# Performance work log

Measured on AMD Instinct MI355X. Metric: run time of the kernel, lower is better.

## Reference

```python
import jax, jax.numpy as jnp
import numpy as np

B, L, S, D, H, DH = 32, 96, 96, 512, 8, 64  # d_ff = S*S = 9216


def setup_inputs() -> dict:
    key = jax.random.key(0)
    ks = jax.random.split(key, 13)
    sc = 0.02
    inp = {
        "queries": jax.random.normal(ks[0], (B, L, D), jnp.float32),
        "keys": jax.random.normal(ks[1], (B, S, D), jnp.float32),
        "values": jax.random.normal(ks[2], (B, S, D), jnp.float32),
        "attn_mask": jnp.zeros((B, L, S), dtype=bool),
        # projections stored as (in, out); torch Linear is x @ W.T + b
        "Wq": jax.random.normal(ks[3], (D, H * DH), jnp.float32) * sc,
        "bq": jnp.zeros((H * DH,), jnp.float32),
        "Wk": jax.random.normal(ks[4], (D, H * DH), jnp.float32) * sc,
        "bk": jnp.zeros((H * DH,), jnp.float32),
        "Wv": jax.random.normal(ks[5], (D, H * DH), jnp.float32) * sc,
        "bv": jnp.zeros((H * DH,), jnp.float32),
        # core_value initialized as softmax over rank dim, as in the module
        "core": jax.nn.softmax(jax.random.normal(ks[6], (H, DH), jnp.float32), axis=-1),
        "Wo": jax.random.normal(ks[7], (S * S, D), jnp.float32) * sc,
        "bo": jnp.zeros((D,), jnp.float32),
    }
    return inp


def reference(queries, keys, values, attn_mask, Wq, bq, Wk, bk, Wv, bv, core, Wo, bo):
    b, l, _ = queries.shape
    s = keys.shape[1]
    h, d = core.shape
    # NOTE: the original uses .view(H, B, L, -1) on a (B, L, H*d) tensor —
    # a raw reshape, NOT a transpose. Replicate faithfully.
    q = (queries @ Wq + bq).reshape(h, b, l, d)
    k = (keys @ Wk + bk).reshape(h, b, s, d)
    v = (values @ Wv + bv).reshape(h, b, s, d)
    # per-head rank-d CP contraction, summed over heads, averaged by 1/H
    full = jnp.einsum("nh,nbih,nbjh,nbkh->bijk", core, q, k, v) / h  # [B,L,S,S]
    full = full.reshape(b, l, s * s)
    out = full @ Wo + bo  # [B, L, D]
    return out
```

## Files before the change

### kernel.cpp

```cpp
#include <hip/hip_runtime.h>
#include <hip/hip_bf16.h>
#include <stdint.h>

using bf16 = __hip_bfloat16;
typedef float v4f __attribute__((ext_vector_type(4)));
typedef short short8 __attribute__((ext_vector_type(8)));


__device__ __forceinline__ void async_cp16(void* l, const void* g) {
  __builtin_amdgcn_global_load_lds(
      (const __attribute__((address_space(1))) void*)(uintptr_t)g,
      (__attribute__((address_space(3))) void*)(uintptr_t)l, 16, 0, 0);
}

__global__ __launch_bounds__(256) void transpose_f32_bf16(
    const float* __restrict__ src, bf16* __restrict__ dst, int K, int N) {
  __shared__ bf16 T[32][33];
  const int k0 = blockIdx.x * 32, n0 = blockIdx.y * 32;
  const int t = threadIdx.x;
  const int r = t >> 3, c = (t & 7) * 4;
  float4 v = *reinterpret_cast<const float4*>(src + (size_t)(k0 + r) * N + n0 + c);
  T[c + 0][r] = __float2bfloat16(v.x);
  T[c + 1][r] = __float2bfloat16(v.y);
  T[c + 2][r] = __float2bfloat16(v.z);
  T[c + 3][r] = __float2bfloat16(v.w);
  __syncthreads();
  union { uint2 u; bf16 h[4]; } o;
  o.h[0] = T[r][c + 0]; o.h[1] = T[r][c + 1];
  o.h[2] = T[r][c + 2]; o.h[3] = T[r][c + 3];
  *reinterpret_cast<uint2*>(dst + (size_t)(n0 + r) * K + k0 + c) = o.u;
}

#define PJ_LD 72

__global__ __launch_bounds__(256) void proj_mfma(
    const float* __restrict__ X0, const float* __restrict__ X1,
    const float* __restrict__ X2,
    const bf16* __restrict__ WT0, const bf16* __restrict__ WT1,
    const bf16* __restrict__ WT2,
    const float* __restrict__ b0, const float* __restrict__ b1,
    const float* __restrict__ b2, const float* __restrict__ core,
    bf16* __restrict__ O0, bf16* __restrict__ O1, bf16* __restrict__ O2) {
  const int z = blockIdx.z;
  const float* X   = z == 0 ? X0  : (z == 1 ? X1  : X2);
  const bf16* WT   = z == 0 ? WT0 : (z == 1 ? WT1 : WT2);
  const float* bia = z == 0 ? b0  : (z == 1 ? b1  : b2);
  bf16* O          = z == 0 ? O0  : (z == 1 ? O1  : O2);

  __shared__ __align__(16) bf16 As[64 * PJ_LD];
  __shared__ __align__(16) bf16 Bs[64 * PJ_LD];
  const int t = threadIdx.x, w = t >> 6, lane = t & 63;
  const int wr = w >> 1, wc = w & 1, m16 = lane & 15, q = lane >> 4;
  const int bm = blockIdx.x * 64, bn = blockIdx.y * 64;

  v4f acc[2][2] = {};

  for (int k0 = 0; k0 < 512; k0 += 64) {
    __syncthreads();
    #pragma unroll
    for (int c = t; c < 1024; c += 256) {
      const int row = c >> 4, col = (c & 15) * 4;
      float4 v = *reinterpret_cast<const float4*>(
          X + (size_t)(bm + row) * 512 + k0 + col);
      union { uint2 u; bf16 h[4]; } o;
      o.h[0] = __float2bfloat16(v.x); o.h[1] = __float2bfloat16(v.y);
      o.h[2] = __float2bfloat16(v.z); o.h[3] = __float2bfloat16(v.w);
      *reinterpret_cast<uint2*>(&As[row * PJ_LD + col]) = o.u;
    }
    #pragma unroll
    for (int c = t; c < 512; c += 256) {
      const int row = c >> 3, col = (c & 7) * 8;
      *reinterpret_cast<uint4*>(&Bs[row * PJ_LD + col]) =
          *reinterpret_cast<const uint4*>(WT + (size_t)(bn + row) * 512 + k0 + col);
    }
    __syncthreads();

    #pragma unroll
    for (int s = 0; s < 2; s++) {
      const int koff = s * 32 + q * 8;
      short8 af[2], bfr[2];
      #pragma unroll
      for (int mt = 0; mt < 2; mt++)
        af[mt] = *reinterpret_cast<const short8*>(
            &As[(wr * 32 + mt * 16 + m16) * PJ_LD + koff]);
      #pragma unroll
      for (int nt = 0; nt < 2; nt++)
        bfr[nt] = *reinterpret_cast<const short8*>(
            &Bs[(wc * 32 + nt * 16 + m16) * PJ_LD + koff]);
      #pragma unroll
      for (int mt = 0; mt < 2; mt++)
        #pragma unroll
        for (int nt = 0; nt < 2; nt++)
          acc[mt][nt] = __builtin_amdgcn_mfma_f32_16x16x32_bf16(
              af[mt], bfr[nt], acc[mt][nt], 0, 0, 0);
    }
  }

  const bool isQ = (z == 0);
  const int nblk = bm / 384;
  #pragma unroll
  for (int mt = 0; mt < 2; mt++)
    #pragma unroll
    for (int nt = 0; nt < 2; nt++)
      #pragma unroll
      for (int r = 0; r < 4; r++) {
        const int row = bm + wr * 32 + mt * 16 + q * 4 + r;
        const int col = bn + wc * 32 + nt * 16 + m16;
        float v = acc[mt][nt][r] + bia[col];
        if (isQ) v *= core[nblk * 64 + (col & 63)] * 0.125f;
        O[(size_t)row * 512 + col] = __float2bfloat16(v);
      }
}

__global__ __launch_bounds__(256) void stage_b_mfma(
    const bf16* __restrict__ AQ, const bf16* __restrict__ KPb,
    const bf16* __restrict__ VPb, bf16* __restrict__ FULL) {
  const int b = blockIdx.y;
  const int i0 = blockIdx.x * 2;

  __shared__ __align__(16) bf16 smem[19456];
  bf16* Ks0 = smem;
  bf16* Ks1 = smem + 6144;
  bf16* Vs  = smem + 12288;
  bf16* aqs = smem + 18432;

  const int t = threadIdx.x;
  const int w = t >> 6, lane = t & 63;
  const int wr = w >> 1, wc = w & 1;
  const int m16 = lane & 15, q = lane >> 4;
  const int l8 = lane >> 3, l7 = lane & 7;

  if (t < 128) {
    const int isel = t & 1, n = t >> 4, seg = (t >> 1) & 7;
    *reinterpret_cast<uint4*>(&aqs[isel * 512 + n * 64 + seg * 8]) =
        *reinterpret_cast<const uint4*>(
            AQ + (size_t)n * 196608 + b * 6144 + (i0 + isel) * 64 + seg * 8);
  }

  union U8 { uint4 u; bf16 h[8]; };
  const int colq = (t & 7) * 8;
  const int rowk = t >> 3;
  const int krow7 = rowk & 7;

  U8 kk[3];
  {
    const bf16* Kp = KPb + b * 6144;
    #pragma unroll
    for (int c3 = 0; c3 < 3; c3++)
      kk[c3].u = *reinterpret_cast<const uint4*>(Kp + (t + c3 * 256) * 8);
  }

  v4f acc[2][3][3] = {};

  for (int n = 0; n < 8; n++) {
    __syncthreads();
    const bf16* Vp = VPb + (size_t)n * 196608 + b * 6144;
    #pragma unroll
    for (int c = 0; c < 3; c++) {
      const int r0 = (w * 3 + c) * 8;
      async_cp16(&Vs[(w * 3 + c) * 512],
                 Vp + (r0 + l8) * 64 + (l7 ^ l8) * 8);
    }
    float a0f[8], a1f[8];
    {
      U8 a0, a1;
      a0.u = *reinterpret_cast<const uint4*>(&aqs[n * 64 + colq]);
      a1.u = *reinterpret_cast<const uint4*>(&aqs[512 + n * 64 + colq]);
      #pragma unroll
      for (int e = 0; e < 8; e++) {
        a0f[e] = __bfloat162float(a0.h[e]);
        a1f[e] = __bfloat162float(a1.h[e]);
      }
    }
    #pragma unroll
    for (int c3 = 0; c3 < 3; c3++) {
      U8 s0, s1;
      #pragma unroll
      for (int e = 0; e < 8; e++) {
        const float kv = __bfloat162float(kk[c3].h[e]);
        s0.h[e] = __float2bfloat16(kv * a0f[e]);
        s1.h[e] = __float2bfloat16(kv * a1f[e]);
      }
      const int phys = (rowk + 32 * c3) * 64 + (l7 ^ krow7) * 8;
      *reinterpret_cast<uint4*>(&Ks0[phys]) = s0.u;
      *reinterpret_cast<uint4*>(&Ks1[phys]) = s1.u;
    }
    __syncthreads();
    if (n < 7) {
      const bf16* Kp1 = KPb + (size_t)(n + 1) * 196608 + b * 6144;
      #pragma unroll
      for (int c3 = 0; c3 < 3; c3++)
        kk[c3].u = *reinterpret_cast<const uint4*>(Kp1 + (t + c3 * 256) * 8);
    }

    #pragma unroll
    for (int s = 0; s < 2; s++) {
      const int pc = ((s * 4 + q) ^ (m16 & 7)) * 8;
      short8 bfr[3], af0[3], af1[3];
      #pragma unroll
      for (int cc = 0; cc < 3; cc++)
        bfr[cc] = *reinterpret_cast<const short8*>(
            &Vs[(wc * 48 + cc * 16 + m16) * 64 + pc]);
      #pragma unroll
      for (int a = 0; a < 3; a++) {
        af0[a] = *reinterpret_cast<const short8*>(
            &Ks0[(wr * 48 + a * 16 + m16) * 64 + pc]);
        af1[a] = *reinterpret_cast<const short8*>(
            &Ks1[(wr * 48 + a * 16 + m16) * 64 + pc]);
      }
      #pragma unroll
      for (int a = 0; a < 3; a++)
        #pragma unroll
        for (int cc = 0; cc < 3; cc++) {
          acc[0][a][cc] = __builtin_amdgcn_mfma_f32_16x16x32_bf16(
              af0[a], bfr[cc], acc[0][a][cc], 0, 0, 0);
          acc[1][a][cc] = __builtin_amdgcn_mfma_f32_16x16x32_bf16(
              af1[a], bfr[cc], acc[1][a][cc], 0, 0, 0);
        }
    }
  }

  __syncthreads();
  #pragma unroll
  for (int isel = 0; isel < 2; isel++)
    #pragma unroll
    for (int a = 0; a < 3; a++)
      #pragma unroll
      for (int cc = 0; cc < 3; cc++) {
        const int j0 = wr * 48 + a * 16, k0c = wc * 48 + cc * 16;
        #pragma unroll
        for (int r = 0; r < 4; r++)
          smem[isel * 9216 + (j0 + q * 4 + r) * 96 + k0c + m16] =
              __float2bfloat16(acc[isel][a][cc][r]);
      }
  __syncthreads();
  const size_t obase = (size_t)(b * 96 + i0) * 9216;
  #pragma unroll
  for (int c = t; c < 2304; c += 256)
    *reinterpret_cast<uint4*>(FULL + obase + c * 8) =
        *reinterpret_cast<const uint4*>(&smem[c * 8]);
}

__global__ __launch_bounds__(256) void init_out(
    const float* __restrict__ bo, float* __restrict__ out) {
  const int idx = (blockIdx.x * 256 + threadIdx.x) * 4;
  *reinterpret_cast<float4*>(out + idx) =
      *reinterpret_cast<const float4*>(bo + (idx & 511));
}

__global__ __launch_bounds__(256) void stage_c_mfma(
    const bf16* __restrict__ FULL, const bf16* __restrict__ WoT,
    float* __restrict__ out) {
  const int bm = blockIdx.x * 128, bn = blockIdx.y * 64;
  const int kbase = blockIdx.z * 2304;
  __shared__ __align__(16) bf16 As[128 * 128];
  __shared__ __align__(16) bf16 Bs[64 * 128];
  const int t = threadIdx.x;
  const int w = t >> 6, lane = t & 63;
  const int m16 = lane & 15, q = lane >> 4;
  const int l16 = lane >> 4, l15 = lane & 15;

  v4f acc[2][4] = {};

  for (int k0 = kbase; k0 < kbase + 2304; k0 += 128) {
    __syncthreads();
    #pragma unroll
    for (int c = 0; c < 8; c++) {
      const int row = (w * 8 + c) * 4 + l16;
      const int lch = l15 ^ (row & 7);
      async_cp16(&As[(w * 8 + c) * 512],
                 FULL + (size_t)(bm + row) * 9216 + k0 + lch * 8);
    }
    #pragma unroll
    for (int c = 0; c < 4; c++) {
      const int row = (w * 4 + c) * 4 + l16;
      const int lch = l15 ^ (row & 7);
      async_cp16(&Bs[(w * 4 + c) * 512],
                 WoT + (size_t)(bn + row) * 9216 + k0 + lch * 8);
    }
    __syncthreads();

    #pragma unroll
    for (int s = 0; s < 4; s++) {
      const int pc = ((s * 4 + q) ^ (m16 & 7)) * 8;
      short8 af[2], bfr[4];
      #pragma unroll
      for (int mt = 0; mt < 2; mt++)
        af[mt] = *reinterpret_cast<const short8*>(
            &As[(w * 32 + mt * 16 + m16) * 128 + pc]);
      #pragma unroll
      for (int nt = 0; nt < 4; nt++)
        bfr[nt] = *reinterpret_cast<const short8*>(
            &Bs[(nt * 16 + m16) * 128 + pc]);
      #pragma unroll
      for (int mt = 0; mt < 2; mt++)
        #pragma unroll
        for (int nt = 0; nt < 4; nt++)
          acc[mt][nt] = __builtin_amdgcn_mfma_f32_16x16x32_bf16(
              af[mt], bfr[nt], acc[mt][nt], 0, 0, 0);
    }
  }

  #pragma unroll
  for (int mt = 0; mt < 2; mt++)
    #pragma unroll
    for (int nt = 0; nt < 4; nt++)
      #pragma unroll
      for (int r = 0; r < 4; r++) {
        const int row = bm + w * 32 + mt * 16 + q * 4 + r;
        const int col = bn + nt * 16 + m16;
        atomicAdd(&out[(size_t)row * 512 + col], acc[mt][nt][r]);
      }
}

extern "C" void kernel_launch(void* const* d_in, const int* in_sizes, int n_in,
                              void* d_out, int out_size, void* d_ws, size_t ws_size,
                              hipStream_t stream) {
  const float* queries = (const float*)d_in[0];
  const float* keys    = (const float*)d_in[1];
  const float* values  = (const float*)d_in[2];
  const float* Wq   = (const float*)d_in[4];
  const float* bq   = (const float*)d_in[5];
  const float* Wk   = (const float*)d_in[6];
  const float* bk   = (const float*)d_in[7];
  const float* Wv   = (const float*)d_in[8];
  const float* bv   = (const float*)d_in[9];
  const float* core = (const float*)d_in[10];
  const float* Wo   = (const float*)d_in[11];
  const float* bo   = (const float*)d_in[12];
  float* out = (float*)d_out;

  char* ws = (char*)d_ws;
  bf16* AQb = (bf16*)(ws);
  bf16* KPb = (bf16*)(ws + 3145728);
  bf16* VPb = (bf16*)(ws + 6291456);
  bf16* WTq = (bf16*)(ws + 9437184);
  bf16* WTk = (bf16*)(ws + 9961472);
  bf16* WTv = (bf16*)(ws + 10485760);
  bf16* WoT = (bf16*)(ws + 11010048);
  bf16* FULL = (bf16*)(ws + 20447232);

  const dim3 blk(256);

  transpose_f32_bf16<<<dim3(16, 16),  blk, 0, stream>>>(Wq, WTq, 512, 512);
  transpose_f32_bf16<<<dim3(16, 16),  blk, 0, stream>>>(Wk, WTk, 512, 512);
  transpose_f32_bf16<<<dim3(16, 16),  blk, 0, stream>>>(Wv, WTv, 512, 512);
  transpose_f32_bf16<<<dim3(288, 16), blk, 0, stream>>>(Wo, WoT, 9216, 512);

  proj_mfma<<<dim3(48, 8, 3), blk, 0, stream>>>(
      queries, keys, values, WTq, WTk, WTv, bq, bk, bv, core, AQb, KPb, VPb);

  stage_b_mfma<<<dim3(48, 32), blk, 0, stream>>>(AQb, KPb, VPb, FULL);

  init_out<<<dim3(1536), blk, 0, stream>>>(bo, out);
  stage_c_mfma<<<dim3(24, 8, 4), blk, 0, stream>>>(FULL, WoT, out);
}
```

Before: 224.0 us.

## Fuse QKV weight transposes into projection, restructure stage B and stage C tiling

Three separate weight-transpose launches are removed: the projection kernel now reads fp32 W directly and transposes into shared memory while converting to bf16. Stage B now builds the scaled-K tiles for two heads per barrier pair, reads V fragments straight from global memory into registers instead of through LDS, and sets an occupancy hint of 3 blocks. Stage C moves to 128x128 output tiles with a 64-wide K step and an 8-way K split. This trades fewer launches and barriers for more register pressure, uncoalesced scalar LDS stores in the projection, and more atomics in stage C.

```diff
diff --git a/kernel.cpp b/kernel.cpp
--- a/kernel.cpp
+++ b/kernel.cpp
@@ -36,16 +36,16 @@
 __global__ __launch_bounds__(256) void proj_mfma(
     const float* __restrict__ X0, const float* __restrict__ X1,
     const float* __restrict__ X2,
-    const bf16* __restrict__ WT0, const bf16* __restrict__ WT1,
-    const bf16* __restrict__ WT2,
+    const float* __restrict__ W0, const float* __restrict__ W1,
+    const float* __restrict__ W2,
     const float* __restrict__ b0, const float* __restrict__ b1,
     const float* __restrict__ b2, const float* __restrict__ core,
     bf16* __restrict__ O0, bf16* __restrict__ O1, bf16* __restrict__ O2) {
   const int z = blockIdx.z;
-  const float* X   = z == 0 ? X0  : (z == 1 ? X1  : X2);
-  const bf16* WT   = z == 0 ? WT0 : (z == 1 ? WT1 : WT2);
-  const float* bia = z == 0 ? b0  : (z == 1 ? b1  : b2);
-  bf16* O          = z == 0 ? O0  : (z == 1 ? O1  : O2);
+  const float* X   = z == 0 ? X0 : (z == 1 ? X1 : X2);
+  const float* W   = z == 0 ? W0 : (z == 1 ? W1 : W2);
+  const float* bia = z == 0 ? b0 : (z == 1 ? b1 : b2);
+  bf16* O          = z == 0 ? O0 : (z == 1 ? O1 : O2);
 
   __shared__ __align__(16) bf16 As[64 * PJ_LD];
   __shared__ __align__(16) bf16 Bs[64 * PJ_LD];
@@ -68,10 +68,14 @@
       *reinterpret_cast<uint2*>(&As[row * PJ_LD + col]) = o.u;
     }
     #pragma unroll
-    for (int c = t; c < 512; c += 256) {
-      const int row = c >> 3, col = (c & 7) * 8;
-      *reinterpret_cast<uint4*>(&Bs[row * PJ_LD + col]) =
-          *reinterpret_cast<const uint4*>(WT + (size_t)(bn + row) * 512 + k0 + col);
+    for (int c = t; c < 1024; c += 256) {
+      const int kr = c >> 4, nc = (c & 15) * 4;
+      float4 v = *reinterpret_cast<const float4*>(
+          W + (size_t)(k0 + kr) * 512 + bn + nc);
+      Bs[(nc + 0) * PJ_LD + kr] = __float2bfloat16(v.x);
+      Bs[(nc + 1) * PJ_LD + kr] = __float2bfloat16(v.y);
+      Bs[(nc + 2) * PJ_LD + kr] = __float2bfloat16(v.z);
+      Bs[(nc + 3) * PJ_LD + kr] = __float2bfloat16(v.w);
     }
     __syncthreads();
 
@@ -112,188 +116,189 @@
       }
 }
 
-__global__ __launch_bounds__(256) void stage_b_mfma(
+__global__ __launch_bounds__(256, 3) void stage_b_mfma(
     const bf16* __restrict__ AQ, const bf16* __restrict__ KPb,
     const bf16* __restrict__ VPb, bf16* __restrict__ FULL) {
   const int b = blockIdx.y;
   const int i0 = blockIdx.x * 2;
 
-  __shared__ __align__(16) bf16 smem[19456];
-  bf16* Ks0 = smem;
-  bf16* Ks1 = smem + 6144;
-  bf16* Vs  = smem + 12288;
-  bf16* aqs = smem + 18432;
-
+  __shared__ __align__(16) bf16 smem[25600];
+  bf16* aqs = smem + 24576;
+
+  const int t = threadIdx.x;
+  const int w = t >> 6, lane = t & 63;
+  const int wr = w >> 1, wc = w & 1;
+  const int m16 = lane & 15, q = lane >> 4;
+
+  if (t < 128) {
+    const int isel = t & 1, n = t >> 4, seg = (t >> 1) & 7;
+    *reinterpret_cast<uint4*>(&aqs[isel * 512 + n * 64 + seg * 8]) =
+        *reinterpret_cast<const uint4*>(
+            AQ + (size_t)n * 196608 + b * 6144 + (i0 + isel) * 64 + seg * 8);
+  }
+
+  union U8 { uint4 u; bf16 h[8]; };
+  const int colq = (t & 7) * 8;
+  const int rowk = t >> 3;
+  const int krow7 = rowk & 7;
+
+  U8 kk[2][3];
+  #pragma unroll
+  for (int nn = 0; nn < 2; nn++) {
+    const bf16* Kp = KPb + (size_t)nn * 196608 + b * 6144;
+    #pragma unroll
+    for (int c3 = 0; c3 < 3; c3++)
+      kk[nn][c3].u = *reinterpret_cast<const uint4*>(Kp + (t + c3 * 256) * 8);
+  }
+
+  v4f acc[2][3][3] = {};
+
+  for (int np = 0; np < 4; np++) {
+    __syncthreads();
+    #pragma unroll
+    for (int nn = 0; nn < 2; nn++) {
+      const int n = np * 2 + nn;
+      U8 a0, a1;
+      a0.u = *reinterpret_cast<const uint4*>(&aqs[n * 64 + colq]);
+      a1.u = *reinterpret_cast<const uint4*>(&aqs[512 + n * 64 + colq]);
+      bf16* Ks0 = smem + (0 * 2 + nn) * 6144;
+      bf16* Ks1 = smem + (1 * 2 + nn) * 6144;
+      #pragma unroll
+      for (int c3 = 0; c3 < 3; c3++) {
+        U8 s0, s1;
+        #pragma unroll
+        for (int e = 0; e < 8; e++) {
+          const float kv = __bfloat162float(kk[nn][c3].h[e]);
+          s0.h[e] = __float2bfloat16(kv * __bfloat162float(a0.h[e]));
+          s1.h[e] = __float2bfloat16(kv * __bfloat162float(a1.h[e]));
+        }
+        const int phys = (rowk + 32 * c3) * 64 + (colq / 8 ^ krow7) * 8;
+        *reinterpret_cast<uint4*>(&Ks0[phys]) = s0.u;
+        *reinterpret_cast<uint4*>(&Ks1[phys]) = s1.u;
+      }
+    }
+    __syncthreads();
+    if (np < 3) {
+      #pragma unroll
+      for (int nn = 0; nn < 2; nn++) {
+        const bf16* Kp = KPb + (size_t)(np * 2 + 2 + nn) * 196608 + b * 6144;
+        #pragma unroll
+        for (int c3 = 0; c3 < 3; c3++)
+          kk[nn][c3].u =
+              *reinterpret_cast<const uint4*>(Kp + (t + c3 * 256) * 8);
+      }
+    }
+
+    #pragma unroll
+    for (int nn = 0; nn < 2; nn++) {
+      const bf16* Vp = VPb + (size_t)(np * 2 + nn) * 196608 + b * 6144;
+      const bf16* Ks0 = smem + nn * 6144;
+      const bf16* Ks1 = smem + (2 + nn) * 6144;
+      uint4 vf[2][3];
+      #pragma unroll
+      for (int s = 0; s < 2; s++)
+        #pragma unroll
+        for (int cc = 0; cc < 3; cc++)
+          vf[s][cc] = *reinterpret_cast<const uint4*>(
+              Vp + (wc * 48 + cc * 16 + m16) * 64 + s * 32 + q * 8);
+      #pragma unroll
+      for (int s = 0; s < 2; s++) {
+        const int pc = ((s * 4 + q) ^ (m16 & 7)) * 8;
+        short8 af0[3], af1[3];
+        #pragma unroll
+        for (int a = 0; a < 3; a++) {
+          af0[a] = *reinterpret_cast<const short8*>(
+              &Ks0[(wr * 48 + a * 16 + m16) * 64 + pc]);
+          af1[a] = *reinterpret_cast<const short8*>(
+              &Ks1[(wr * 48 + a * 16 + m16) * 64 + pc]);
+        }
+        #pragma unroll
+        for (int a = 0; a < 3; a++)
+          #pragma unroll
+          for (int cc = 0; cc < 3; cc++) {
+            const short8 bv = *reinterpret_cast<const short8*>(&vf[s][cc]);
+            acc[0][a][cc] = __builtin_amdgcn_mfma_f32_16x16x32_bf16(
+                af0[a], bv, acc[0][a][cc], 0, 0, 0);
+            acc[1][a][cc] = __builtin_amdgcn_mfma_f32_16x16x32_bf16(
+                af1[a], bv, acc[1][a][cc], 0, 0, 0);
+          }
+      }
+    }
+  }
+
+  __syncthreads();
+  #pragma unroll
+  for (int isel = 0; isel < 2; isel++)
+    #pragma unroll
+    for (int a = 0; a < 3; a++)
+      #pragma unroll
+      for (int cc = 0; cc < 3; cc++) {
+        const int j0 = wr * 48 + a * 16, k0c = wc * 48 + cc * 16;
+        #pragma unroll
+        for (int r = 0; r < 4; r++)
+          smem[isel * 9216 + (j0 + q * 4 + r) * 96 + k0c + m16] =
+              __float2bfloat16(acc[isel][a][cc][r]);
+      }
+  __syncthreads();
+  const size_t obase = (size_t)(b * 96 + i0) * 9216;
+  #pragma unroll
+  for (int c = t; c < 2304; c += 256)
+    *reinterpret_cast<uint4*>(FULL + obase + c * 8) =
+        *reinterpret_cast<const uint4*>(&smem[c * 8]);
+}
+
+__global__ __launch_bounds__(256) void init_out(
+    const float* __restrict__ bo, float* __restrict__ out) {
+  const int idx = (blockIdx.x * 256 + threadIdx.x) * 4;
+  *reinterpret_cast<float4*>(out + idx) =
+      *reinterpret_cast<const float4*>(bo + (idx & 511));
+}
+
+__global__ __launch_bounds__(256) void stage_c_mfma(
+    const bf16* __restrict__ FULL, const bf16* __restrict__ WoT,
+    float* __restrict__ out) {
+  const int bm = blockIdx.x * 128, bn = blockIdx.y * 128;
+  const int kbase = blockIdx.z * 1152;
+  __shared__ __align__(16) bf16 As[128 * 64];
+  __shared__ __align__(16) bf16 Bs[128 * 64];
   const int t = threadIdx.x;
   const int w = t >> 6, lane = t & 63;
   const int wr = w >> 1, wc = w & 1;
   const int m16 = lane & 15, q = lane >> 4;
   const int l8 = lane >> 3, l7 = lane & 7;
 
-  if (t < 128) {
-    const int isel = t & 1, n = t >> 4, seg = (t >> 1) & 7;
-    *reinterpret_cast<uint4*>(&aqs[isel * 512 + n * 64 + seg * 8]) =
-        *reinterpret_cast<const uint4*>(
-            AQ + (size_t)n * 196608 + b * 6144 + (i0 + isel) * 64 + seg * 8);
-  }
-
-  union U8 { uint4 u; bf16 h[8]; };
-  const int colq = (t & 7) * 8;
-  const int rowk = t >> 3;
-  const int krow7 = rowk & 7;
-
-  U8 kk[3];
-  {
-    const bf16* Kp = KPb + b * 6144;
-    #pragma unroll
-    for (int c3 = 0; c3 < 3; c3++)
-      kk[c3].u = *reinterpret_cast<const uint4*>(Kp + (t + c3 * 256) * 8);
-  }
-
-  v4f acc[2][3][3] = {};
-
-  for (int n = 0; n < 8; n++) {
-    __syncthreads();
-    const bf16* Vp = VPb + (size_t)n * 196608 + b * 6144;
-    #pragma unroll
-    for (int c = 0; c < 3; c++) {
-      const int r0 = (w * 3 + c) * 8;
-      async_cp16(&Vs[(w * 3 + c) * 512],
-                 Vp + (r0 + l8) * 64 + (l7 ^ l8) * 8);
-    }
-    float a0f[8], a1f[8];
-    {
-      U8 a0, a1;
-      a0.u = *reinterpret_cast<const uint4*>(&aqs[n * 64 + colq]);
-      a1.u = *reinterpret_cast<const uint4*>(&aqs[512 + n * 64 + colq]);
-      #pragma unroll
-      for (int e = 0; e < 8; e++) {
-        a0f[e] = __bfloat162float(a0.h[e]);
-        a1f[e] = __bfloat162float(a1.h[e]);
-      }
-    }
-    #pragma unroll
-    for (int c3 = 0; c3 < 3; c3++) {
-      U8 s0, s1;
-      #pragma unroll
-      for (int e = 0; e < 8; e++) {
-        const float kv = __bfloat162float(kk[c3].h[e]);
-        s0.h[e] = __float2bfloat16(kv * a0f[e]);
-        s1.h[e] = __float2bfloat16(kv * a1f[e]);
-      }
-      const int phys = (rowk + 32 * c3) * 64 + (l7 ^ krow7) * 8;
-      *reinterpret_cast<uint4*>(&Ks0[phys]) = s0.u;
-      *reinterpret_cast<uint4*>(&Ks1[phys]) = s1.u;
-    }
-    __syncthreads();
-    if (n < 7) {
-      const bf16* Kp1 = KPb + (size_t)(n + 1) * 196608 + b * 6144;
-      #pragma unroll
-      for (int c3 = 0; c3 < 3; c3++)
-        kk[c3].u = *reinterpret_cast<const uint4*>(Kp1 + (t + c3 * 256) * 8);
-    }
+  v4f acc[4][4] = {};
+
+  for (int k0 = kbase; k0 < kbase + 1152; k0 += 64) {
+    __syncthreads();
+    #pragma unroll
+    for (int c = 0; c < 4; c++) {
+      const int row = w * 32 + c * 8 + l8;
+      async_cp16(&As[(w * 4 + c) * 512],
+                 FULL + (size_t)(bm + row) * 9216 + k0 + (l7 ^ l8) * 8);
+    }
+    #pragma unroll
+    for (int c = 0; c < 4; c++) {
+      const int row = w * 32 + c * 8 + l8;
+      async_cp16(&Bs[(w * 4 + c) * 512],
+                 WoT + (size_t)(bn + row) * 9216 + k0 + (l7 ^ l8) * 8);
+    }
+    __syncthreads();
 
     #pragma unroll
     for (int s = 0; s < 2; s++) {
       const int pc = ((s * 4 + q) ^ (m16 & 7)) * 8;
-      short8 bfr[3], af0[3], af1[3];
-      #pragma unroll
-      for (int cc = 0; cc < 3; cc++)
-        bfr[cc] = *reinterpret_cast<const short8*>(
-            &Vs[(wc * 48 + cc * 16 + m16) * 64 + pc]);
-      #pragma unroll
-      for (int a = 0; a < 3; a++) {
-        af0[a] = *reinterpret_cast<const short8*>(
-            &Ks0[(wr * 48 + a * 16 + m16) * 64 + pc]);
-        af1[a] = *reinterpret_cast<const short8*>(
-            &Ks1[(wr * 48 + a * 16 + m16) * 64 + pc]);
-      }
-      #pragma unroll
-      for (int a = 0; a < 3; a++)
-        #pragma unroll
-        for (int cc = 0; cc < 3; cc++) {
-          acc[0][a][cc] = __builtin_amdgcn_mfma_f32_16x16x32_bf16(
-              af0[a], bfr[cc], acc[0][a][cc], 0, 0, 0);
-          acc[1][a][cc] = __builtin_amdgcn_mfma_f32_16x16x32_bf16(
-              af1[a], bfr[cc], acc[1][a][cc], 0, 0, 0);
-        }
-    }
-  }
-
-  __syncthreads();
-  #pragma unroll
-  for (int isel = 0; isel < 2; isel++)
-    #pragma unroll
-    for (int a = 0; a < 3; a++)
-      #pragma unroll
-      for (int cc = 0; cc < 3; cc++) {
-        const int j0 = wr * 48 + a * 16, k0c = wc * 48 + cc * 16;
-        #pragma unroll
-        for (int r = 0; r < 4; r++)
-          smem[isel * 9216 + (j0 + q * 4 + r) * 96 + k0c + m16] =
-              __float2bfloat16(acc[isel][a][cc][r]);
-      }
-  __syncthreads();
-  const size_t obase = (size_t)(b * 96 + i0) * 9216;
-  #pragma unroll
-  for (int c = t; c < 2304; c += 256)
-    *reinterpret_cast<uint4*>(FULL + obase + c * 8) =
-        *reinterpret_cast<const uint4*>(&smem[c * 8]);
-}
-
-__global__ __launch_bounds__(256) void init_out(
-    const float* __restrict__ bo, float* __restrict__ out) {
-  const int idx = (blockIdx.x * 256 + threadIdx.x) * 4;
-  *reinterpret_cast<float4*>(out + idx) =
-      *reinterpret_cast<const float4*>(bo + (idx & 511));
-}
-
-__global__ __launch_bounds__(256) void stage_c_mfma(
-    const bf16* __restrict__ FULL, const bf16* __restrict__ WoT,
-    float* __restrict__ out) {
-  const int bm = blockIdx.x * 128, bn = blockIdx.y * 64;
-  const int kbase = blockIdx.z * 2304;
-  __shared__ __align__(16) bf16 As[128 * 128];
-  __shared__ __align__(16) bf16 Bs[64 * 128];
-  const int t = threadIdx.x;
-  const int w = t >> 6, lane = t & 63;
-  const int m16 = lane & 15, q = lane >> 4;
-  const int l16 = lane >> 4, l15 = lane & 15;
-
-  v4f acc[2][4] = {};
-
-  for (int k0 = kbase; k0 < kbase + 2304; k0 += 128) {
-    __syncthreads();
-    #pragma unroll
-    for (int c = 0; c < 8; c++) {
-      const int row = (w * 8 + c) * 4 + l16;
-      const int lch = l15 ^ (row & 7);
-      async_cp16(&As[(w * 8 + c) * 512],
-                 FULL + (size_t)(bm + row) * 9216 + k0 + lch * 8);
-    }
-    #pragma unroll
-    for (int c = 0; c < 4; c++) {
-      const int row = (w * 4 + c) * 4 + l16;
-      const int lch = l15 ^ (row & 7);
-      async_cp16(&Bs[(w * 4 + c) * 512],
-                 WoT + (size_t)(bn + row) * 9216 + k0 + lch * 8);
-    }
-    __syncthreads();
-
-    #pragma unroll
-    for (int s = 0; s < 4; s++) {
-      const int pc = ((s * 4 + q) ^ (m16 & 7)) * 8;
-      short8 af[2], bfr[4];
-      #pragma unroll
-      for (int mt = 0; mt < 2; mt++)
+      short8 af[4], bfr[4];
+      #pragma unroll
+      for (int mt = 0; mt < 4; mt++)
         af[mt] = *reinterpret_cast<const short8*>(
-            &As[(w * 32 + mt * 16 + m16) * 128 + pc]);
+            &As[(wr * 64 + mt * 16 + m16) * 64 + pc]);
       #pragma unroll
       for (int nt = 0; nt < 4; nt++)
         bfr[nt] = *reinterpret_cast<const short8*>(
-            &Bs[(nt * 16 + m16) * 128 + pc]);
-      #pragma unroll
-      for (int mt = 0; mt < 2; mt++)
+            &Bs[(wc * 64 + nt * 16 + m16) * 64 + pc]);
+      #pragma unroll
+      for (int mt = 0; mt < 4; mt++)
         #pragma unroll
         for (int nt = 0; nt < 4; nt++)
           acc[mt][nt] = __builtin_amdgcn_mfma_f32_16x16x32_bf16(
@@ -302,13 +307,13 @@
   }
 
   #pragma unroll
-  for (int mt = 0; mt < 2; mt++)
+  for (int mt = 0; mt < 4; mt++)
     #pragma unroll
     for (int nt = 0; nt < 4; nt++)
       #pragma unroll
       for (int r = 0; r < 4; r++) {
-        const int row = bm + w * 32 + mt * 16 + q * 4 + r;
-        const int col = bn + nt * 16 + m16;
+        const int row = bm + wr * 64 + mt * 16 + q * 4 + r;
+        const int col = bn + wc * 64 + nt * 16 + m16;
         atomicAdd(&out[(size_t)row * 512 + col], acc[mt][nt][r]);
       }
 }
@@ -334,24 +339,18 @@
   bf16* AQb = (bf16*)(ws);
   bf16* KPb = (bf16*)(ws + 3145728);
   bf16* VPb = (bf16*)(ws + 6291456);
-  bf16* WTq = (bf16*)(ws + 9437184);
-  bf16* WTk = (bf16*)(ws + 9961472);
-  bf16* WTv = (bf16*)(ws + 10485760);
-  bf16* WoT = (bf16*)(ws + 11010048);
-  bf16* FULL = (bf16*)(ws + 20447232);
+  bf16* WoT = (bf16*)(ws + 9437184);
+  bf16* FULL = (bf16*)(ws + 18874368);
 
   const dim3 blk(256);
 
-  transpose_f32_bf16<<<dim3(16, 16),  blk, 0, stream>>>(Wq, WTq, 512, 512);
-  transpose_f32_bf16<<<dim3(16, 16),  blk, 0, stream>>>(Wk, WTk, 512, 512);
-  transpose_f32_bf16<<<dim3(16, 16),  blk, 0, stream>>>(Wv, WTv, 512, 512);
   transpose_f32_bf16<<<dim3(288, 16), blk, 0, stream>>>(Wo, WoT, 9216, 512);
 
   proj_mfma<<<dim3(48, 8, 3), blk, 0, stream>>>(
-      queries, keys, values, WTq, WTk, WTv, bq, bk, bv, core, AQb, KPb, VPb);
+      queries, keys, values, Wq, Wk, Wv, bq, bk, bv, core, AQb, KPb, VPb);
 
   stage_b_mfma<<<dim3(48, 32), blk, 0, stream>>>(AQb, KPb, VPb, FULL);
 
   init_out<<<dim3(1536), blk, 0, stream>>>(bo, out);
-  stage_c_mfma<<<dim3(24, 8, 4), blk, 0, stream>>>(FULL, WoT, out);
-}
+  stage_c_mfma<<<dim3(24, 4, 8), blk, 0, stream>>>(FULL, WoT, out);
+}
```

After: 257.9 us. +15.1%, slower.
